# Performance work log

Measured on AMD Instinct MI355X. Metric: run time of the kernel, lower is better.

The kernel has to match this reference:

```python
import jax, jax.numpy as jnp
import numpy as np

HEADS = 8
DIM_HEAD = 64
MAX_REL = 200  # max_rel_dist


def setup_inputs() -> dict:
    key = jax.random.key(0)
    ks = jax.random.split(key, 5)
    B, N, D = 4, 2048, 512
    x = jax.random.normal(ks[0], (B, N, D), dtype=jnp.float32)
    temporal_mask = jax.random.randint(ks[1], (N, N), 0, 2, dtype=jnp.int32)
    gamma = jnp.ones((D,), jnp.float32)
    beta = jnp.zeros((D,), jnp.float32)
    Wqkv = jax.random.normal(ks[2], (D, 3 * HEADS * DIM_HEAD), dtype=jnp.float32) * 0.02
    Wout = jax.random.normal(ks[3], (HEADS * DIM_HEAD, D), dtype=jnp.float32) * 0.02
    bout = jnp.zeros((D,), jnp.float32)
    rel_table = jax.random.normal(ks[4], (2 * MAX_REL - 1,), dtype=jnp.float32) * 0.02
    return {"x": x, "gamma": gamma, "beta": beta, "Wqkv": Wqkv, "Wout": Wout,
            "bout": bout, "rel_table": rel_table, "temporal_mask": temporal_mask}


def reference(x, gamma, beta, Wqkv, Wout, bout, rel_table, temporal_mask):
    B, N, D = x.shape
    scale = DIM_HEAD ** -0.5
    # LayerNorm
    mu = jnp.mean(x, axis=-1, keepdims=True)
    var = jnp.mean(jnp.square(x - mu), axis=-1, keepdims=True)
    xn = (x - mu) * jax.lax.rsqrt(var + 1e-5) * gamma + beta
    # QKV projection (no bias), split heads: b n (h d) -> b h n d
    qkv = xn @ Wqkv  # [B, N, 3*H*d]
    q, k, v = jnp.split(qkv, 3, axis=-1)
    split = lambda t: t.reshape(B, N, HEADS, DIM_HEAD).transpose(0, 2, 1, 3)
    q, k, v = split(q), split(k), split(v)
    # scores with learned relative-position bias
    dots = jnp.einsum('bhnd,bhmd->bhnm', q, k) * scale  # [B,H,N,N]
    idx = jnp.arange(N)
    rel = jnp.clip(idx[:, None] - idx[None, :], -(MAX_REL - 1), MAX_REL - 1) + MAX_REL - 1
    dots = dots + rel_table[rel][None, None, :, :]
    # temporal mask (0 -> -inf); large negative for grad safety
    dots = jnp.where(temporal_mask[None, None, :, :] == 0, jnp.float32(-1e9), dots)
    attn = jax.nn.softmax(dots, axis=-1)
    out = jnp.einsum('bhnm,bhmd->bhnd', attn, v)
    out = out.transpose(0, 2, 1, 3).reshape(B, N, HEADS * DIM_HEAD)
    return out @ Wout + bout
```

## Files before the change

### kernel.cpp

```cpp
#include <hip/hip_runtime.h>

typedef __attribute__((ext_vector_type(8))) short bf16x8;
typedef __attribute__((ext_vector_type(4))) short bf16x4;
typedef __attribute__((ext_vector_type(4))) float f32x4;
typedef unsigned short ushort_t;

#define B_ 4
#define H_ 8
#define N_ 2048
#define D_ 512
#define MAXREL 199

__device__ __forceinline__ ushort_t f2bf(float f) {
    union { float f; unsigned u; } v; v.f = f;
    unsigned r = v.u + 0x7fffu + ((v.u >> 16) & 1u);
    return (ushort_t)(r >> 16);
}
__device__ __forceinline__ ushort_t f2bf_fast(float f) {
    union { float f; unsigned u; } v; v.f = f;
    return (ushort_t)((v.u + 0x8000u) >> 16);
}
__device__ __forceinline__ float bf2f(ushort_t u) {
    union { unsigned u; float f; } v; v.u = ((unsigned)u) << 16;
    return v.f;
}
__device__ __forceinline__ void gl_lds16(const ushort_t* g, ushort_t* l) {
    __builtin_amdgcn_global_load_lds(
        (const __attribute__((address_space(1))) void*)g,
        (__attribute__((address_space(3))) void*)l,
        16, 0, 0);
}

#define PREP_BIAS  16384
#define PREP_LN    8192
#define PREP_WQ    768
#define PREP_WO    256
__global__ __launch_bounds__(256) void prep_kernel(const float* __restrict__ x,
                                                   const float* __restrict__ gamma,
                                                   const float* __restrict__ beta,
                                                   ushort_t* __restrict__ xn,
                                                   const float* __restrict__ Wqkv,
                                                   ushort_t* __restrict__ WqkvT,
                                                   const float* __restrict__ Wout,
                                                   ushort_t* __restrict__ WoutT,
                                                   const float* __restrict__ rel,
                                                   const int* __restrict__ mask,
                                                   ushort_t* __restrict__ bp) {
    __shared__ float smem[32 * 33];
    const int blk = blockIdx.x;
    const int t = threadIdx.x;

    if (blk < PREP_BIAS) {
        int idx = blk * 256 + t;
        int n = idx >> 11, m = idx & 2047;
        int dl = n - m;
        dl = dl < -MAXREL ? -MAXREL : (dl > MAXREL ? MAXREL : dl);
        float v = (mask[idx] == 0) ? -1e9f : rel[dl + MAXREL];
        int jt = m >> 6, m16 = m & 15, nt = (m >> 4) & 3;
        bp[((size_t)n * 32 + jt) * 64 + m16 * 4 + nt] = f2bf(v);
    } else if (blk < PREP_BIAS + PREP_LN) {
        const int row = blk - PREP_BIAS;
        const float* xr = x + (size_t)row * D_;
        float v0 = xr[t];
        float v1 = xr[t + 256];
        float s = v0 + v1;
        for (int o = 32; o > 0; o >>= 1) s += __shfl_down(s, o);
        if ((t & 63) == 0) smem[t >> 6] = s;
        __syncthreads();
        float mu = (smem[0] + smem[1] + smem[2] + smem[3]) * (1.0f / D_);
        __syncthreads();
        float d0 = v0 - mu, d1 = v1 - mu;
        float s2 = d0 * d0 + d1 * d1;
        for (int o = 32; o > 0; o >>= 1) s2 += __shfl_down(s2, o);
        if ((t & 63) == 0) smem[t >> 6] = s2;
        __syncthreads();
        float var = (smem[0] + smem[1] + smem[2] + smem[3]) * (1.0f / D_);
        float rs = rsqrtf(var + 1e-5f);
        ushort_t* yr = xn + (size_t)row * D_;
        yr[t]       = f2bf(d0 * rs * gamma[t]       + beta[t]);
        yr[t + 256] = f2bf(d1 * rs * gamma[t + 256] + beta[t + 256]);
    } else {
        const float* W; ushort_t* Wt; int Nn, i;
        if (blk < PREP_BIAS + PREP_LN + PREP_WQ) {
            i = blk - (PREP_BIAS + PREP_LN); W = Wqkv; Wt = WqkvT; Nn = 1536;
        } else {
            i = blk - (PREP_BIAS + PREP_LN + PREP_WQ); W = Wout; Wt = WoutT; Nn = 512;
        }
        const int nb = Nn >> 5;
        const int bx = (i % nb) * 32, by = (i / nb) * 32;
        const int tx = t & 31, ty = t >> 5;
        float (*tile)[33] = (float(*)[33])smem;
        #pragma unroll
        for (int k = 0; k < 32; k += 8)
            tile[ty + k][tx] = W[(size_t)(by + ty + k) * Nn + bx + tx];
        __syncthreads();
        #pragma unroll
        for (int k = 0; k < 32; k += 8)
            Wt[(size_t)(bx + ty + k) * 512 + by + tx] = f2bf(tile[tx][ty + k]);
    }
}

__global__ __launch_bounds__(256) void gemm_qkv(const ushort_t* __restrict__ A,
                                                const ushort_t* __restrict__ Bt,
                                                ushort_t* __restrict__ qb,
                                                ushort_t* __restrict__ kb,
                                                ushort_t* __restrict__ vb) {
    __shared__ ushort_t As[128 * 32];
    __shared__ ushort_t Bs[128 * 32];
    const int t = threadIdx.x;
    const int lane = t & 63, w = t >> 6;
    const int m16 = lane & 15, quad = lane >> 4;
    const int wr = w >> 1, wc = w & 1;
    const int r0 = blockIdx.y * 128, c0 = blockIdx.x * 128;

    const ushort_t* Ag = A  + (size_t)(r0 + (t >> 2)) * D_ + (t & 3) * 8;
    const ushort_t* Bg = Bt + (size_t)(c0 + (t >> 2)) * D_ + (t & 3) * 8;
    ushort_t* AsW = As + w * 512;
    ushort_t* BsW = Bs + w * 512;

    f32x4 acc[4][4];
    #pragma unroll
    for (int i = 0; i < 4; i++)
        #pragma unroll
        for (int j = 0; j < 4; j++) acc[i][j] = (f32x4){0.f, 0.f, 0.f, 0.f};

    for (int k0 = 0; k0 < D_; k0 += 32) {
        gl_lds16(Ag + k0, AsW);
        gl_lds16(Ag + k0 + (size_t)64 * D_, AsW + 2048);
        gl_lds16(Bg + k0, BsW);
        gl_lds16(Bg + k0 + (size_t)64 * D_, BsW + 2048);
        __syncthreads();
        bf16x8 af[4], bfr[4];
        #pragma unroll
        for (int rt = 0; rt < 4; rt++)
            af[rt] = *(const bf16x8*)(As + (wr * 64 + rt * 16 + m16) * 32 + quad * 8);
        #pragma unroll
        for (int ct = 0; ct < 4; ct++)
            bfr[ct] = *(const bf16x8*)(Bs + (wc * 64 + ct * 16 + m16) * 32 + quad * 8);
        #pragma unroll
        for (int rt = 0; rt < 4; rt++)
            #pragma unroll
            for (int ct = 0; ct < 4; ct++)
                acc[rt][ct] = __builtin_amdgcn_mfma_f32_16x16x32_bf16(af[rt], bfr[ct], acc[rt][ct], 0, 0, 0);
        __syncthreads();
    }

    #pragma unroll
    for (int ct = 0; ct < 4; ct++) {
        int cc = c0 + wc * 64 + ct * 16;
        int which = cc >> 9;
        int h = (cc >> 6) & 7;
        int d = (cc & 63) + m16;
        #pragma unroll
        for (int rt = 0; rt < 4; rt++) {
            int rowb = r0 + wr * 64 + rt * 16 + quad * 4;
            int b = rowb >> 11, n0 = rowb & 2047;
            if (which == 0) {
                #pragma unroll
                for (int r = 0; r < 4; r++)
                    qb[((size_t)((b * H_ + h) * N_ + n0 + r)) * 64 + d] = f2bf(acc[rt][ct][r] * 0.125f);
            } else if (which == 1) {
                #pragma unroll
                for (int r = 0; r < 4; r++)
                    kb[((size_t)((b * H_ + h) * N_ + n0 + r)) * 64 + d] = f2bf(acc[rt][ct][r]);
            } else {
                union { ushort_t u4[4]; unsigned long long ll; } pk;
                #pragma unroll
                for (int r = 0; r < 4; r++) pk.u4[r] = f2bf(acc[rt][ct][r]);
                *(unsigned long long*)(vb + ((size_t)((b * H_ + h) * 64 + d)) * N_ + n0) = pk.ll;
            }
        }
    }
}

__global__ __launch_bounds__(256) void gemm_out(const ushort_t* __restrict__ A,
                                                const ushort_t* __restrict__ Bt,
                                                const float* __restrict__ bias,
                                                float* __restrict__ C) {
    __shared__ ushort_t As[64 * 32];
    __shared__ ushort_t Bs[128 * 32];
    const int t = threadIdx.x;
    const int lane = t & 63, w = t >> 6;
    const int m16 = lane & 15, quad = lane >> 4;
    const int wr = w >> 1, wc = w & 1;
    const int r0 = blockIdx.y * 64, c0 = blockIdx.x * 128;

    const ushort_t* Ag = A  + (size_t)(r0 + (t >> 2)) * D_ + (t & 3) * 8;
    const ushort_t* Bg = Bt + (size_t)(c0 + (t >> 2)) * D_ + (t & 3) * 8;
    ushort_t* AsW = As + w * 512;
    ushort_t* BsW = Bs + w * 512;

    f32x4 acc[2][4];
    #pragma unroll
    for (int i = 0; i < 2; i++)
        #pragma unroll
        for (int j = 0; j < 4; j++) acc[i][j] = (f32x4){0.f, 0.f, 0.f, 0.f};

    for (int k0 = 0; k0 < D_; k0 += 32) {
        gl_lds16(Ag + k0, AsW);
        gl_lds16(Bg + k0, BsW);
        gl_lds16(Bg + k0 + (size_t)64 * D_, BsW + 2048);
        __syncthreads();
        bf16x8 af[2], bfr[4];
        #pragma unroll
        for (int mf = 0; mf < 2; mf++)
            af[mf] = *(const bf16x8*)(As + (wr * 32 + mf * 16 + m16) * 32 + quad * 8);
        #pragma unroll
        for (int nt = 0; nt < 4; nt++)
            bfr[nt] = *(const bf16x8*)(Bs + (wc * 64 + nt * 16 + m16) * 32 + quad * 8);
        #pragma unroll
        for (int mf = 0; mf < 2; mf++)
            #pragma unroll
            for (int nt = 0; nt < 4; nt++)
                acc[mf][nt] = __builtin_amdgcn_mfma_f32_16x16x32_bf16(af[mf], bfr[nt], acc[mf][nt], 0, 0, 0);
        __syncthreads();
    }

    #pragma unroll
    for (int mf = 0; mf < 2; mf++) {
        #pragma unroll
        for (int nt = 0; nt < 4; nt++) {
            int col = c0 + wc * 64 + nt * 16 + m16;
            int row0 = r0 + wr * 32 + mf * 16 + quad * 4;
            float bv = bias[col];
            #pragma unroll
            for (int r = 0; r < 4; r++)
                C[(size_t)(row0 + r) * 512 + col] = acc[mf][nt][r] + bv;
        }
    }
}

__global__ __launch_bounds__(512, 4) void attn_mfma(const ushort_t* __restrict__ qb,
                                                    const ushort_t* __restrict__ kb,
                                                    const ushort_t* __restrict__ vb,
                                                    const ushort_t* __restrict__ bp,
                                                    ushort_t* __restrict__ attn) {
    __shared__ ushort_t Ks[2][64 * 64];
    __shared__ ushort_t Vs[2][64 * 64];
    __shared__ ushort_t p_s[8][16 * 64];

    const int t = threadIdx.x;
    const int w = t >> 6, lane = t & 63;
    const int m16 = lane & 15, quad = lane >> 4;
    const int id = blockIdx.x;
    const int bh = id & 31;
    const int qt = id >> 5;
    const int b = bh >> 3, h = bh & 7;
    const int n0w = qt * 128 + w * 16;

    const int srow = t >> 3, scb = t & 7;
    const int soff = srow * 64 + (scb ^ (srow & 7)) * 8;
    const ushort_t* kgbase = kb + ((size_t)bh * N_) * 64;
    const ushort_t* vgbase = vb + ((size_t)bh * 64) * N_;

    const ushort_t* qpb = qb + ((size_t)(bh * N_ + n0w + m16)) * 64 + quad * 8;
    bf16x8 qa0 = *(const bf16x8*)(qpb);
    bf16x8 qa1 = *(const bf16x8*)(qpb + 32);

    *(bf16x8*)(&Ks[0][soff]) = *(const bf16x8*)(kgbase + (size_t)srow * 64 + scb * 8);
    *(bf16x8*)(&Vs[0][soff]) = *(const bf16x8*)(vgbase + (size_t)srow * N_ + scb * 8);
    __syncthreads();

    f32x4 o[4];
    #pragma unroll
    for (int nt = 0; nt < 4; nt++) o[nt] = (f32x4){0.f, 0.f, 0.f, 0.f};
    float rsum[4] = {};

    for (int jt = 0; jt < 32; jt++) {
        const int buf = jt & 1;
        const int j0 = jt * 64;
        const bool more = (jt < 31);

        bf16x8 kst, vst;
        if (more) {
            kst = *(const bf16x8*)(kgbase + (size_t)(j0 + 64 + srow) * 64 + scb * 8);
            vst = *(const bf16x8*)(vgbase + (size_t)srow * N_ + j0 + 64 + scb * 8);
        }

        bf16x4 bcur[4];
        #pragma unroll
        for (int r = 0; r < 4; r++) {
            int n = n0w + quad * 4 + r;
            bcur[r] = *(const bf16x4*)(bp + ((size_t)n * 32 + jt) * 64 + m16 * 4);
        }

        f32x4 s[4];
        #pragma unroll
        for (int nt = 0; nt < 4; nt++) {
            int kr = nt * 16 + m16;
            bf16x8 kf0 = *(const bf16x8*)(&Ks[buf][kr * 64 + ((quad) ^ (kr & 7)) * 8]);
            bf16x8 kf1 = *(const bf16x8*)(&Ks[buf][kr * 64 + ((quad + 4) ^ (kr & 7)) * 8]);
            f32x4 a2 = (f32x4){0.f, 0.f, 0.f, 0.f};
            a2 = __builtin_amdgcn_mfma_f32_16x16x32_bf16(qa0, kf0, a2, 0, 0, 0);
            a2 = __builtin_amdgcn_mfma_f32_16x16x32_bf16(qa1, kf1, a2, 0, 0, 0);
            s[nt] = a2;
        }

        ushort_t* pw = p_s[w];
        #pragma unroll
        for (int nt = 0; nt < 4; nt++) {
            int chunk = nt * 2 + (m16 >> 3), pos = m16 & 7;
            #pragma unroll
            for (int r = 0; r < 4; r++) {
                float p = __expf(s[nt][r] + bf2f((ushort_t)bcur[r][nt]));
                rsum[r] += p;
                int row = quad * 4 + r;
                pw[row * 64 + ((chunk ^ (row & 7)) << 3) + pos] = f2bf_fast(p);
            }
        }

        bf16x8 pa0 = *(const bf16x8*)(pw + m16 * 64 + ((quad ^ (m16 & 7)) << 3));
        bf16x8 pa1 = *(const bf16x8*)(pw + m16 * 64 + (((quad + 4) ^ (m16 & 7)) << 3));

        #pragma unroll
        for (int nt = 0; nt < 4; nt++) {
            int d = nt * 16 + m16;
            bf16x8 vf0 = *(const bf16x8*)(&Vs[buf][d * 64 + ((quad) ^ (d & 7)) * 8]);
            bf16x8 vf1 = *(const bf16x8*)(&Vs[buf][d * 64 + ((quad + 4) ^ (d & 7)) * 8]);
            o[nt] = __builtin_amdgcn_mfma_f32_16x16x32_bf16(pa0, vf0, o[nt], 0, 0, 0);
            o[nt] = __builtin_amdgcn_mfma_f32_16x16x32_bf16(pa1, vf1, o[nt], 0, 0, 0);
        }

        if (more) {
            *(bf16x8*)(&Ks[buf ^ 1][soff]) = kst;
            *(bf16x8*)(&Vs[buf ^ 1][soff]) = vst;
        }
        __syncthreads();
    }

    #pragma unroll
    for (int r = 0; r < 4; r++) {
        float t2 = rsum[r];
        t2 += __shfl_xor(t2, 1);
        t2 += __shfl_xor(t2, 2);
        t2 += __shfl_xor(t2, 4);
        t2 += __shfl_xor(t2, 8);
        float inv = 1.0f / t2;
        int n = n0w + quad * 4 + r;
        ushort_t* orow = attn + ((size_t)(b * N_ + n)) * 512 + h * 64 + m16;
        #pragma unroll
        for (int nt = 0; nt < 4; nt++) orow[nt * 16] = f2bf(o[nt][r] * inv);
    }
}

extern "C" void kernel_launch(void* const* d_in, const int* in_sizes, int n_in,
                              void* d_out, int out_size, void* d_ws, size_t ws_size,
                              hipStream_t stream) {
    const float* x     = (const float*)d_in[0];
    const float* gamma = (const float*)d_in[1];
    const float* beta  = (const float*)d_in[2];
    const float* Wqkv  = (const float*)d_in[3];
    const float* Wout  = (const float*)d_in[4];
    const float* bout  = (const float*)d_in[5];
    const float* rel   = (const float*)d_in[6];
    const int*   mask  = (const int*)d_in[7];
    float* out = (float*)d_out;

    char* wsb = (char*)d_ws;
    ushort_t* xn    = (ushort_t*)(wsb);
    ushort_t* attnb = (ushort_t*)(wsb + ( 8u << 20));
    ushort_t* qb    = (ushort_t*)(wsb + (16u << 20));
    ushort_t* kb    = (ushort_t*)(wsb + (24u << 20));
    ushort_t* vb    = (ushort_t*)(wsb + (32u << 20));
    ushort_t* WqkvT = (ushort_t*)(wsb + (40u << 20));
    ushort_t* WoutT = (ushort_t*)(wsb + (42u << 20));
    ushort_t* bp    = (ushort_t*)(wsb + (44u << 20));

    prep_kernel<<<PREP_BIAS + PREP_LN + PREP_WQ + PREP_WO, 256, 0, stream>>>(
        x, gamma, beta, xn, Wqkv, WqkvT, Wout, WoutT, rel, mask, bp);

    gemm_qkv<<<dim3(1536 / 128, 8192 / 128), 256, 0, stream>>>(xn, WqkvT, qb, kb, vb);

    attn_mfma<<<512, 512, 0, stream>>>(qb, kb, vb, bp, attnb);

    gemm_out<<<dim3(512 / 128, 8192 / 64), 256, 0, stream>>>(attnb, WoutT, bout, out);
}
```

Measured before the change: 200.4 us.

## Pass attention probabilities via lane shuffles instead of LDS, shrink blocks

The score MFMA now computes the transposed tile (K as the A operand), so each lane holds four consecutive key columns for a single query row. The bf16 probabilities are then packed into 64-bit words and redistributed across lanes with shuffles to form the A operand of the PV MFMA, removing the per-wave LDS round trip for P. The bias/mask table is stored row-major and read contiguously, and the row-sum reduction is reorganised to match the new layout. Blocks shrink from 512 to 256 threads (64 queries each), which doubles the grid and makes every thread stage two K/V rows per tile; this also doubles total K/V traffic from global memory.

```diff
diff --git a/kernel.cpp b/kernel.cpp
--- a/kernel.cpp
+++ b/kernel.cpp
@@ -4,6 +4,7 @@
 typedef __attribute__((ext_vector_type(4))) short bf16x4;
 typedef __attribute__((ext_vector_type(4))) float f32x4;
 typedef unsigned short ushort_t;
+typedef unsigned long long u64_t;
 
 #define B_ 4
 #define H_ 8
@@ -56,8 +57,7 @@
         int dl = n - m;
         dl = dl < -MAXREL ? -MAXREL : (dl > MAXREL ? MAXREL : dl);
         float v = (mask[idx] == 0) ? -1e9f : rel[dl + MAXREL];
-        int jt = m >> 6, m16 = m & 15, nt = (m >> 4) & 3;
-        bp[((size_t)n * 32 + jt) * 64 + m16 * 4 + nt] = f2bf(v);
+        bp[idx] = f2bf(v);
     } else if (blk < PREP_BIAS + PREP_LN) {
         const int row = blk - PREP_BIAS;
         const float* xr = x + (size_t)row * D_;
@@ -230,14 +230,13 @@
     }
 }
 
-__global__ __launch_bounds__(512, 4) void attn_mfma(const ushort_t* __restrict__ qb,
+__global__ __launch_bounds__(256, 4) void attn_mfma(const ushort_t* __restrict__ qb,
                                                     const ushort_t* __restrict__ kb,
                                                     const ushort_t* __restrict__ vb,
                                                     const ushort_t* __restrict__ bp,
                                                     ushort_t* __restrict__ attn) {
     __shared__ ushort_t Ks[2][64 * 64];
     __shared__ ushort_t Vs[2][64 * 64];
-    __shared__ ushort_t p_s[8][16 * 64];
 
     const int t = threadIdx.x;
     const int w = t >> 6, lane = t & 63;
@@ -246,10 +245,16 @@
     const int bh = id & 31;
     const int qt = id >> 5;
     const int b = bh >> 3, h = bh & 7;
-    const int n0w = qt * 128 + w * 16;
-
-    const int srow = t >> 3, scb = t & 7;
-    const int soff = srow * 64 + (scb ^ (srow & 7)) * 8;
+    const int n0w = qt * 64 + w * 16;
+
+    const int srcA = ((2 * quad) & 3) * 16 + m16;
+    const int srcB = ((2 * quad + 1) & 3) * 16 + m16;
+    const bool selHi = (quad >> 1) != 0;
+
+    const int srow0 = t >> 3, scb = t & 7;
+    const int srow1 = srow0 + 32;
+    const int soff0 = srow0 * 64 + (scb ^ (srow0 & 7)) * 8;
+    const int soff1 = srow1 * 64 + (scb ^ (srow1 & 7)) * 8;
     const ushort_t* kgbase = kb + ((size_t)bh * N_) * 64;
     const ushort_t* vgbase = vb + ((size_t)bh * 64) * N_;
 
@@ -257,32 +262,38 @@
     bf16x8 qa0 = *(const bf16x8*)(qpb);
     bf16x8 qa1 = *(const bf16x8*)(qpb + 32);
 
-    *(bf16x8*)(&Ks[0][soff]) = *(const bf16x8*)(kgbase + (size_t)srow * 64 + scb * 8);
-    *(bf16x8*)(&Vs[0][soff]) = *(const bf16x8*)(vgbase + (size_t)srow * N_ + scb * 8);
+    const ushort_t* bprow = bp + (size_t)(n0w + m16) * 2048;
+
+    *(bf16x8*)(&Ks[0][soff0]) = *(const bf16x8*)(kgbase + (size_t)srow0 * 64 + scb * 8);
+    *(bf16x8*)(&Ks[0][soff1]) = *(const bf16x8*)(kgbase + (size_t)srow1 * 64 + scb * 8);
+    *(bf16x8*)(&Vs[0][soff0]) = *(const bf16x8*)(vgbase + (size_t)srow0 * N_ + scb * 8);
+    *(bf16x8*)(&Vs[0][soff1]) = *(const bf16x8*)(vgbase + (size_t)srow1 * N_ + scb * 8);
     __syncthreads();
 
     f32x4 o[4];
     #pragma unroll
     for (int nt = 0; nt < 4; nt++) o[nt] = (f32x4){0.f, 0.f, 0.f, 0.f};
-    float rsum[4] = {};
+    float rsum = 0.f;
 
     for (int jt = 0; jt < 32; jt++) {
         const int buf = jt & 1;
         const int j0 = jt * 64;
         const bool more = (jt < 31);
 
-        bf16x8 kst, vst;
+        bf16x8 kst0, kst1, vst0, vst1;
         if (more) {
-            kst = *(const bf16x8*)(kgbase + (size_t)(j0 + 64 + srow) * 64 + scb * 8);
-            vst = *(const bf16x8*)(vgbase + (size_t)srow * N_ + j0 + 64 + scb * 8);
+            const ushort_t* kg = kgbase + (size_t)(j0 + 64) * 64;
+            const ushort_t* vg = vgbase + (j0 + 64);
+            kst0 = *(const bf16x8*)(kg + (size_t)srow0 * 64 + scb * 8);
+            kst1 = *(const bf16x8*)(kg + (size_t)srow1 * 64 + scb * 8);
+            vst0 = *(const bf16x8*)(vg + (size_t)srow0 * N_ + scb * 8);
+            vst1 = *(const bf16x8*)(vg + (size_t)srow1 * N_ + scb * 8);
         }
 
         bf16x4 bcur[4];
         #pragma unroll
-        for (int r = 0; r < 4; r++) {
-            int n = n0w + quad * 4 + r;
-            bcur[r] = *(const bf16x4*)(bp + ((size_t)n * 32 + jt) * 64 + m16 * 4);
-        }
+        for (int nt = 0; nt < 4; nt++)
+            bcur[nt] = *(const bf16x4*)(bprow + j0 + nt * 16 + quad * 4);
 
         f32x4 s[4];
         #pragma unroll
@@ -291,52 +302,62 @@
             bf16x8 kf0 = *(const bf16x8*)(&Ks[buf][kr * 64 + ((quad) ^ (kr & 7)) * 8]);
             bf16x8 kf1 = *(const bf16x8*)(&Ks[buf][kr * 64 + ((quad + 4) ^ (kr & 7)) * 8]);
             f32x4 a2 = (f32x4){0.f, 0.f, 0.f, 0.f};
-            a2 = __builtin_amdgcn_mfma_f32_16x16x32_bf16(qa0, kf0, a2, 0, 0, 0);
-            a2 = __builtin_amdgcn_mfma_f32_16x16x32_bf16(qa1, kf1, a2, 0, 0, 0);
+            a2 = __builtin_amdgcn_mfma_f32_16x16x32_bf16(kf0, qa0, a2, 0, 0, 0);
+            a2 = __builtin_amdgcn_mfma_f32_16x16x32_bf16(kf1, qa1, a2, 0, 0, 0);
             s[nt] = a2;
         }
 
-        ushort_t* pw = p_s[w];
+        u64_t pk[4];
         #pragma unroll
         for (int nt = 0; nt < 4; nt++) {
-            int chunk = nt * 2 + (m16 >> 3), pos = m16 & 7;
+            union { ushort_t u4[4]; u64_t ll; } pkk;
             #pragma unroll
             for (int r = 0; r < 4; r++) {
-                float p = __expf(s[nt][r] + bf2f((ushort_t)bcur[r][nt]));
-                rsum[r] += p;
-                int row = quad * 4 + r;
-                pw[row * 64 + ((chunk ^ (row & 7)) << 3) + pos] = f2bf_fast(p);
+                float p = __expf(s[nt][r] + bf2f((ushort_t)bcur[nt][r]));
+                rsum += p;
+                pkk.u4[r] = f2bf_fast(p);
             }
-        }
-
-        bf16x8 pa0 = *(const bf16x8*)(pw + m16 * 64 + ((quad ^ (m16 & 7)) << 3));
-        bf16x8 pa1 = *(const bf16x8*)(pw + m16 * 64 + (((quad + 4) ^ (m16 & 7)) << 3));
+            pk[nt] = pkk.ll;
+        }
+
+        bf16x8 pa[2];
+        #pragma unroll
+        for (int g = 0; g < 2; g++) {
+            u64_t lo0 = __shfl(pk[2 * g],     srcA);
+            u64_t hi0 = __shfl(pk[2 * g + 1], srcA);
+            u64_t lo1 = __shfl(pk[2 * g],     srcB);
+            u64_t hi1 = __shfl(pk[2 * g + 1], srcB);
+            union { u64_t u2[2]; bf16x8 v; } af;
+            af.u2[0] = selHi ? hi0 : lo0;
+            af.u2[1] = selHi ? hi1 : lo1;
+            pa[g] = af.v;
+        }
 
         #pragma unroll
         for (int nt = 0; nt < 4; nt++) {
             int d = nt * 16 + m16;
             bf16x8 vf0 = *(const bf16x8*)(&Vs[buf][d * 64 + ((quad) ^ (d & 7)) * 8]);
             bf16x8 vf1 = *(const bf16x8*)(&Vs[buf][d * 64 + ((quad + 4) ^ (d & 7)) * 8]);
-            o[nt] = __builtin_amdgcn_mfma_f32_16x16x32_bf16(pa0, vf0, o[nt], 0, 0, 0);
-            o[nt] = __builtin_amdgcn_mfma_f32_16x16x32_bf16(pa1, vf1, o[nt], 0, 0, 0);
+            o[nt] = __builtin_amdgcn_mfma_f32_16x16x32_bf16(pa[0], vf0, o[nt], 0, 0, 0);
+            o[nt] = __builtin_amdgcn_mfma_f32_16x16x32_bf16(pa[1], vf1, o[nt], 0, 0, 0);
         }
 
         if (more) {
-            *(bf16x8*)(&Ks[buf ^ 1][soff]) = kst;
-            *(bf16x8*)(&Vs[buf ^ 1][soff]) = vst;
-        }
-        __syncthreads();
-    }
-
+            *(bf16x8*)(&Ks[buf ^ 1][soff0]) = kst0;
+            *(bf16x8*)(&Ks[buf ^ 1][soff1]) = kst1;
+            *(bf16x8*)(&Vs[buf ^ 1][soff0]) = vst0;
+            *(bf16x8*)(&Vs[buf ^ 1][soff1]) = vst1;
+        }
+        __syncthreads();
+    }
+
+    float r1 = rsum + __shfl_xor(rsum, 16);
+    float rsumF = r1 + __shfl_xor(r1, 32);
     #pragma unroll
     for (int r = 0; r < 4; r++) {
-        float t2 = rsum[r];
-        t2 += __shfl_xor(t2, 1);
-        t2 += __shfl_xor(t2, 2);
-        t2 += __shfl_xor(t2, 4);
-        t2 += __shfl_xor(t2, 8);
-        float inv = 1.0f / t2;
-        int n = n0w + quad * 4 + r;
+        int qloc = quad * 4 + r;
+        float inv = 1.0f / __shfl(rsumF, qloc);
+        int n = n0w + qloc;
         ushort_t* orow = attn + ((size_t)(b * N_ + n)) * 512 + h * 64 + m16;
         #pragma unroll
         for (int nt = 0; nt < 4; nt++) orow[nt * 16] = f2bf(o[nt][r] * inv);
@@ -371,7 +392,7 @@
 
     gemm_qkv<<<dim3(1536 / 128, 8192 / 128), 256, 0, stream>>>(xn, WqkvT, qb, kb, vb);
 
-    attn_mfma<<<512, 512, 0, stream>>>(qb, kb, vb, bp, attnb);
+    attn_mfma<<<1024, 256, 0, stream>>>(qb, kb, vb, bp, attnb);
 
     gemm_out<<<dim3(512 / 128, 8192 / 64), 256, 0, stream>>>(attnb, WoutT, bout, out);
 }
```

New measurement: 224.5 us. 12.0% more time.

## Transpose score MFMA, store bias row-major, use exp2 with folded log2e

Applied to the files above, without the earlier changes.

Swaps the QK^T MFMA operands so each lane holds scores for a single query row. This lets the bias be read as contiguous row-major bf16x4 chunks, P be written to padded LDS with 64-bit stores, and the row sum be kept as one scalar per lane that is reduced across quads at the end. It also folds log2(e) into the Q scale and the bias so the softmax can use exp2f instead of __expf. The aim is fewer scattered LDS stores, fewer shuffles and cheaper exponentials, at the cost of a different bias layout and LDS padding.

```diff
diff --git a/kernel.cpp b/kernel.cpp
--- a/kernel.cpp
+++ b/kernel.cpp
@@ -4,12 +4,14 @@
 typedef __attribute__((ext_vector_type(4))) short bf16x4;
 typedef __attribute__((ext_vector_type(4))) float f32x4;
 typedef unsigned short ushort_t;
+typedef unsigned long long u64_t;
 
 #define B_ 4
 #define H_ 8
 #define N_ 2048
 #define D_ 512
 #define MAXREL 199
+#define LOG2E 1.44269504f
 
 __device__ __forceinline__ ushort_t f2bf(float f) {
     union { float f; unsigned u; } v; v.f = f;
@@ -56,8 +58,7 @@
         int dl = n - m;
         dl = dl < -MAXREL ? -MAXREL : (dl > MAXREL ? MAXREL : dl);
         float v = (mask[idx] == 0) ? -1e9f : rel[dl + MAXREL];
-        int jt = m >> 6, m16 = m & 15, nt = (m >> 4) & 3;
-        bp[((size_t)n * 32 + jt) * 64 + m16 * 4 + nt] = f2bf(v);
+        bp[idx] = f2bf(v * LOG2E);
     } else if (blk < PREP_BIAS + PREP_LN) {
         const int row = blk - PREP_BIAS;
         const float* xr = x + (size_t)row * D_;
@@ -158,7 +159,7 @@
             if (which == 0) {
                 #pragma unroll
                 for (int r = 0; r < 4; r++)
-                    qb[((size_t)((b * H_ + h) * N_ + n0 + r)) * 64 + d] = f2bf(acc[rt][ct][r] * 0.125f);
+                    qb[((size_t)((b * H_ + h) * N_ + n0 + r)) * 64 + d] = f2bf(acc[rt][ct][r] * (0.125f * LOG2E));
             } else if (which == 1) {
                 #pragma unroll
                 for (int r = 0; r < 4; r++)
@@ -237,7 +238,7 @@
                                                     ushort_t* __restrict__ attn) {
     __shared__ ushort_t Ks[2][64 * 64];
     __shared__ ushort_t Vs[2][64 * 64];
-    __shared__ ushort_t p_s[8][16 * 64];
+    __shared__ ushort_t p_t[8][16 * 72];
 
     const int t = threadIdx.x;
     const int w = t >> 6, lane = t & 63;
@@ -257,6 +258,8 @@
     bf16x8 qa0 = *(const bf16x8*)(qpb);
     bf16x8 qa1 = *(const bf16x8*)(qpb + 32);
 
+    const ushort_t* bprow = bp + (size_t)(n0w + m16) * 2048;
+
     *(bf16x8*)(&Ks[0][soff]) = *(const bf16x8*)(kgbase + (size_t)srow * 64 + scb * 8);
     *(bf16x8*)(&Vs[0][soff]) = *(const bf16x8*)(vgbase + (size_t)srow * N_ + scb * 8);
     __syncthreads();
@@ -264,7 +267,9 @@
     f32x4 o[4];
     #pragma unroll
     for (int nt = 0; nt < 4; nt++) o[nt] = (f32x4){0.f, 0.f, 0.f, 0.f};
-    float rsum[4] = {};
+    float rsum = 0.f;
+
+    ushort_t* pw = p_t[w];
 
     for (int jt = 0; jt < 32; jt++) {
         const int buf = jt & 1;
@@ -279,10 +284,8 @@
 
         bf16x4 bcur[4];
         #pragma unroll
-        for (int r = 0; r < 4; r++) {
-            int n = n0w + quad * 4 + r;
-            bcur[r] = *(const bf16x4*)(bp + ((size_t)n * 32 + jt) * 64 + m16 * 4);
-        }
+        for (int nt = 0; nt < 4; nt++)
+            bcur[nt] = *(const bf16x4*)(bprow + j0 + nt * 16 + quad * 4);
 
         f32x4 s[4];
         #pragma unroll
@@ -291,26 +294,25 @@
             bf16x8 kf0 = *(const bf16x8*)(&Ks[buf][kr * 64 + ((quad) ^ (kr & 7)) * 8]);
             bf16x8 kf1 = *(const bf16x8*)(&Ks[buf][kr * 64 + ((quad + 4) ^ (kr & 7)) * 8]);
             f32x4 a2 = (f32x4){0.f, 0.f, 0.f, 0.f};
-            a2 = __builtin_amdgcn_mfma_f32_16x16x32_bf16(qa0, kf0, a2, 0, 0, 0);
-            a2 = __builtin_amdgcn_mfma_f32_16x16x32_bf16(qa1, kf1, a2, 0, 0, 0);
+            a2 = __builtin_amdgcn_mfma_f32_16x16x32_bf16(kf0, qa0, a2, 0, 0, 0);
+            a2 = __builtin_amdgcn_mfma_f32_16x16x32_bf16(kf1, qa1, a2, 0, 0, 0);
             s[nt] = a2;
         }
 
-        ushort_t* pw = p_s[w];
         #pragma unroll
         for (int nt = 0; nt < 4; nt++) {
-            int chunk = nt * 2 + (m16 >> 3), pos = m16 & 7;
+            union { ushort_t u4[4]; u64_t ll; } pkk;
             #pragma unroll
             for (int r = 0; r < 4; r++) {
-                float p = __expf(s[nt][r] + bf2f((ushort_t)bcur[r][nt]));
-                rsum[r] += p;
-                int row = quad * 4 + r;
-                pw[row * 64 + ((chunk ^ (row & 7)) << 3) + pos] = f2bf_fast(p);
+                float p = exp2f(s[nt][r] + bf2f((ushort_t)bcur[nt][r]));
+                rsum += p;
+                pkk.u4[r] = f2bf_fast(p);
             }
-        }
-
-        bf16x8 pa0 = *(const bf16x8*)(pw + m16 * 64 + ((quad ^ (m16 & 7)) << 3));
-        bf16x8 pa1 = *(const bf16x8*)(pw + m16 * 64 + (((quad + 4) ^ (m16 & 7)) << 3));
+            *(u64_t*)(&pw[m16 * 72 + nt * 16 + quad * 4]) = pkk.ll;
+        }
+
+        bf16x8 pa0 = *(const bf16x8*)(&pw[m16 * 72 + quad * 8]);
+        bf16x8 pa1 = *(const bf16x8*)(&pw[m16 * 72 + 32 + quad * 8]);
 
         #pragma unroll
         for (int nt = 0; nt < 4; nt++) {
@@ -328,15 +330,13 @@
         __syncthreads();
     }
 
+    float r1 = rsum + __shfl_xor(rsum, 16);
+    float rsumF = r1 + __shfl_xor(r1, 32);
     #pragma unroll
     for (int r = 0; r < 4; r++) {
-        float t2 = rsum[r];
-        t2 += __shfl_xor(t2, 1);
-        t2 += __shfl_xor(t2, 2);
-        t2 += __shfl_xor(t2, 4);
-        t2 += __shfl_xor(t2, 8);
-        float inv = 1.0f / t2;
-        int n = n0w + quad * 4 + r;
+        int qloc = quad * 4 + r;
+        float inv = 1.0f / __shfl(rsumF, qloc);
+        int n = n0w + qloc;
         ushort_t* orow = attn + ((size_t)(b * N_ + n)) * 512 + h * 64 + m16;
         #pragma unroll
         for (int nt = 0; nt < 4; nt++) orow[nt * 16] = f2bf(o[nt][r] * inv);
```

Result: slower. 214.4 us (+7.0%).
